# Kernel optimization log

Measured on AMD Instinct MI355X. Metric: run time of the kernel, lower is better.

Reference implementation:

```python
import jax, jax.numpy as jnp
import numpy as np

B, N, C, H = 8, 4096, 768, 8
EPS = 1e-12  # F.normalize eps


def setup_inputs() -> dict:
    key = jax.random.key(0)
    k1, k2, k3, k4 = jax.random.split(key, 4)
    x = jax.random.normal(k1, (B, N, C), dtype=jnp.float32)
    Wqkv = jax.random.normal(k2, (C, 3 * C), dtype=jnp.float32) * (1.0 / np.sqrt(C))
    temperature = jnp.ones((H, 1, 1), dtype=jnp.float32)
    Wproj = jax.random.normal(k3, (C, C), dtype=jnp.float32) * (1.0 / np.sqrt(C))
    bproj = jax.random.normal(k4, (C,), dtype=jnp.float32) * 0.01
    return {"x": x, "Wqkv": Wqkv, "temperature": temperature, "Wproj": Wproj, "bproj": bproj}


def _l2norm(t):
    # F.normalize(dim=-1): t / max(||t||_2, eps)
    n = jnp.sqrt(jnp.sum(t * t, axis=-1, keepdims=True))
    return t / jnp.maximum(n, EPS)


def reference(x, Wqkv, temperature, Wproj, bproj):
    b, n, c = x.shape
    h = temperature.shape[0]
    hd = c // h
    qkv = x @ Wqkv  # [B, N, 3C]
    qkv = qkv.reshape(b, n, 3, h, hd).transpose(2, 0, 3, 4, 1)  # [3, B, H, hd, N]
    q, k, v = qkv[0], qkv[1], qkv[2]
    q = _l2norm(q)  # normalize over token dim N
    k = _l2norm(k)
    # channel-channel attention: [B, H, hd, hd]
    attn = jnp.einsum('bhdn,bhen->bhde', q, k) * temperature  # temperature [H,1,1] broadcasts
    attn = jax.nn.softmax(attn, axis=-1)
    out = jnp.einsum('bhde,bhen->bhdn', attn, v)  # [B, H, hd, N]
    out = out.transpose(0, 3, 1, 2).reshape(b, n, c)  # [B, N, C]
    return out @ Wproj + bproj
```

## Files before the change

kernel.cpp:

```cpp
#include <hip/hip_runtime.h>
#include <stdint.h>


typedef __attribute__((ext_vector_type(8))) __bf16 bf16x8;
typedef __attribute__((ext_vector_type(4))) float f32x4;

__device__ __forceinline__ unsigned short f2b(float f) {
  uint32_t u = __float_as_uint(f);
  u += 0x7FFF + ((u >> 16) & 1);
  return (unsigned short)(u >> 16);
}

__device__ __forceinline__ void gload16(const void* g, void* l) {
  __builtin_amdgcn_global_load_lds(
      (__attribute__((address_space(1))) void*)(uintptr_t)g,
      (__attribute__((address_space(3))) void*)(uintptr_t)l, 16, 0, 0);
}

__global__ void cvt_bf16(const float* __restrict__ in, unsigned short* __restrict__ out, int n4,
                         float* __restrict__ Z, int nz4) {
  int gid = blockIdx.x * blockDim.x + threadIdx.x;
  if (gid < nz4) reinterpret_cast<float4*>(Z)[gid] = make_float4(0.f, 0.f, 0.f, 0.f);
  int stride = gridDim.x * blockDim.x;
  for (int i = gid; i < n4; i += stride) {
    float4 v = reinterpret_cast<const float4*>(in)[i];
    ushort4 o;
    o.x = f2b(v.x); o.y = f2b(v.y); o.z = f2b(v.z); o.w = f2b(v.w);
    reinterpret_cast<ushort4*>(out)[i] = o;
  }
}

__global__ void cvt_transpose(const float* __restrict__ in, unsigned short* __restrict__ out,
                              int K, int NC) {
  __shared__ float tile[32][33];
  int bx = blockIdx.x, by = blockIdx.y;
  int tx = threadIdx.x & 31, ty = threadIdx.x >> 5;
  for (int r = ty; r < 32; r += 8)
    tile[r][tx] = in[(size_t)(by * 32 + r) * NC + bx * 32 + tx];
  __syncthreads();
  for (int r = ty; r < 32; r += 8)
    out[(size_t)(bx * 32 + r) * K + by * 32 + tx] = f2b(tile[tx][r]);
}


#define BARX() asm volatile("s_barrier" ::: "memory")
#define WAITV(N) asm volatile("s_waitcnt vmcnt(" #N ")" ::: "memory")
#define SCHED() __builtin_amdgcn_sched_barrier(0)

#define STAGE(gbase, p, isB, h, t) do {                                             \
  unsigned short* _lb = &lds[(p)*32768 + (isB)*16384 + (h)*8192 + wid*1024];        \
  const unsigned short* _gb = (gbase) + (size_t)((h)*128 + wid*16)*768 + (t)*64 + lanegoff; \
  gload16(_gb, _lb);                                                                \
  gload16(_gb + 8*768, _lb + 512);                                                  \
} while (0)

#define LOAD_A(p, mh) do {                                                          \
  const unsigned short* _ab = &lds[(p)*32768 + (mh)*8192];                          \
  _Pragma("unroll") for (int _mi = 0; _mi < 4; _mi++)                               \
    _Pragma("unroll") for (int _kk = 0; _kk < 2; _kk++)                             \
      af[_mi][_kk] = *(const bf16x8*)&_ab[(wm*64 + _mi*16 + l16)*64 + ((_kk*4+quad)^(l16&7))*8]; \
} while (0)

#define LOAD_B(dst, p, nh) do {                                                     \
  const unsigned short* _bb = &lds[(p)*32768 + 16384 + (nh)*8192];                  \
  _Pragma("unroll") for (int _ni = 0; _ni < 2; _ni++)                               \
    _Pragma("unroll") for (int _kk = 0; _kk < 2; _kk++)                             \
      dst[_ni][_kk] = *(const bf16x8*)&_bb[(wn*32 + _ni*16 + l16)*64 + ((_kk*4+quad)^(l16&7))*8]; \
} while (0)

#define MFMA_PH(mh, nh, bfx) do {                                                   \
  __builtin_amdgcn_s_setprio(1);                                                    \
  _Pragma("unroll") for (int _m = 0; _m < 4; _m++)                                  \
    _Pragma("unroll") for (int _n = 0; _n < 2; _n++)                                \
      _Pragma("unroll") for (int _k = 0; _k < 2; _k++)                              \
        acc[(mh)*4+_m][(nh)*2+_n] = __builtin_amdgcn_mfma_f32_16x16x32_bf16(        \
            af[_m][_k], bfx[_n][_k], acc[(mh)*4+_m][(nh)*2+_n], 0, 0, 0);           \
  __builtin_amdgcn_s_setprio(0);                                                    \
} while (0)

__global__ __launch_bounds__(512, 2) void gemm_qkv(
    const unsigned short* __restrict__ A, const unsigned short* __restrict__ Bt,
    unsigned short* __restrict__ qkT, unsigned short* __restrict__ vT,
    float* __restrict__ normsq) {
  __shared__ __align__(16) unsigned short lds[65536];
  int lin = blockIdx.y * 9 + blockIdx.x;
  int swz = (lin & 7) * 144 + (lin >> 3);
  int bm = swz / 9;
  int bj = swz - bm * 9;
  int m0 = bm * 256, j0 = bj * 256;
  int tid = threadIdx.x;
  int wid = tid >> 6, lane = tid & 63;
  int wm = wid >> 2, wn = wid & 3;
  int quad = lane >> 4, l16 = lane & 15;
  int srow = lane >> 3, sch = lane & 7;
  int cmem = sch ^ srow;
  int lanegoff = srow * 768 + cmem * 8;

  f32x4 acc[8][4];
  f32x4 z = {0.f, 0.f, 0.f, 0.f};
#pragma unroll
  for (int i = 0; i < 8; i++)
#pragma unroll
    for (int j = 0; j < 4; j++) acc[i][j] = z;

  bf16x8 af[4][2], bf0[2][2], bf1[2][2];

  const unsigned short* Ab2 = A + (size_t)m0 * 768;
  const unsigned short* Bb2 = Bt + (size_t)j0 * 768;

  STAGE(Ab2, 0, 0, 0, 0); STAGE(Bb2, 0, 1, 0, 0); STAGE(Bb2, 0, 1, 1, 0); STAGE(Ab2, 0, 0, 1, 0);
  STAGE(Ab2, 1, 0, 0, 1); STAGE(Bb2, 1, 1, 0, 1); STAGE(Bb2, 1, 1, 1, 1);
  WAITV(10);
  BARX();
  LOAD_A(0, 0);
  LOAD_B(bf0, 0, 0);
  WAITV(8);
  BARX();

  for (int t = 0; t < 10; t++) {
    int p = t & 1;
    LOAD_B(bf1, p, 1);
    STAGE(Ab2, p ^ 1, 0, 1, t + 1);
    BARX(); SCHED();
    MFMA_PH(0, 0, bf0);
    SCHED(); WAITV(8); BARX();
    STAGE(Ab2, p, 0, 0, t + 2);
    BARX(); SCHED();
    MFMA_PH(0, 1, bf1);
    SCHED();
    LOAD_A(p, 1);
    BARX();
    STAGE(Bb2, p, 1, 0, t + 2);
    BARX(); SCHED();
    MFMA_PH(1, 1, bf1);
    SCHED(); WAITV(8); BARX();
    STAGE(Bb2, p, 1, 1, t + 2);
    BARX(); SCHED();
    MFMA_PH(1, 0, bf0);
    SCHED();
    LOAD_A(p ^ 1, 0);
    LOAD_B(bf0, p ^ 1, 0);
    WAITV(8); BARX();
  }
  LOAD_B(bf1, 0, 1);
  STAGE(Ab2, 1, 0, 1, 11);
  BARX(); SCHED(); MFMA_PH(0, 0, bf0); SCHED(); WAITV(8); BARX();
  BARX(); SCHED(); MFMA_PH(0, 1, bf1); SCHED(); LOAD_A(0, 1); BARX();
  BARX(); SCHED(); MFMA_PH(1, 1, bf1); SCHED(); WAITV(4); BARX();
  BARX(); SCHED(); MFMA_PH(1, 0, bf0); SCHED(); LOAD_A(1, 0); LOAD_B(bf0, 1, 0); WAITV(2); BARX();
  LOAD_B(bf1, 1, 1);
  BARX(); SCHED(); MFMA_PH(0, 0, bf0); SCHED(); WAITV(0); BARX();
  BARX(); SCHED(); MFMA_PH(0, 1, bf1); SCHED(); LOAD_A(1, 1); BARX();
  BARX(); SCHED(); MFMA_PH(1, 1, bf1); SCHED(); BARX();
  BARX(); SCHED(); MFMA_PH(1, 0, bf0); SCHED(); BARX();

  int s = bj / 3;
  int b = m0 >> 12;
  int n0 = m0 & 4095;

  if (s < 2) {
#pragma unroll
    for (int ni = 0; ni < 4; ni++) {
      float ss = 0.f;
#pragma unroll
      for (int mi = 0; mi < 8; mi++)
#pragma unroll
        for (int r = 0; r < 4; r++) ss += acc[mi][ni][r] * acc[mi][ni][r];
      ss += __shfl_down(ss, 32, 64);
      ss += __shfl_down(ss, 16, 64);
      if (lane < 16) {
        int cc = (ni >> 1) * 128 + wn * 32 + (ni & 1) * 16 + l16;
        int local = j0 + cc - s * 768;
        int hh = local / 96, d = local - hh * 96;
        atomicAdd(&normsq[s * 6144 + (b * 8 + hh) * 96 + d], ss);
      }
    }
#pragma unroll
    for (int jh = 0; jh < 2; jh++) {
      __syncthreads();
#pragma unroll
      for (int nl = 0; nl < 2; nl++) {
        int ni = jh * 2 + nl;
        int jc = wn * 32 + nl * 16 + l16;
#pragma unroll
        for (int mi = 0; mi < 8; mi++) {
          int mrow = (mi >> 2) * 128 + wm * 64 + (mi & 3) * 16 + quad * 4;
#pragma unroll
          for (int r = 0; r < 4; r++) lds[jc * 264 + mrow + r] = f2b(acc[mi][ni][r]);
        }
      }
      __syncthreads();
#pragma unroll
      for (int it = 0; it < 8; it++) {
        int id = it * 512 + tid;
        int jr = id >> 5, mc = id & 31;
        int j = j0 + jh * 128 + jr;
        int local = j - s * 768;
        int hh = local / 96, d = local - hh * 96;
        size_t off = ((size_t)(s * 64 + b * 8 + hh) * 96 + d) * 4096 + n0 + mc * 8;
        *(uint4*)&qkT[off] = *(const uint4*)&lds[jr * 264 + mc * 8];
      }
    }
  } else {
    int j0v = j0 - 1536;
#pragma unroll
    for (int mh = 0; mh < 2; mh++) {
      __syncthreads();
#pragma unroll
      for (int ml = 0; ml < 4; ml++) {
        int mi = mh * 4 + ml;
        int mloc = wm * 64 + ml * 16 + quad * 4;
#pragma unroll
        for (int ni = 0; ni < 4; ni++) {
          int jc = (ni >> 1) * 128 + wn * 32 + (ni & 1) * 16 + l16;
#pragma unroll
          for (int r = 0; r < 4; r++) lds[(mloc + r) * 264 + jc] = f2b(acc[mi][ni][r]);
        }
      }
      __syncthreads();
#pragma unroll
      for (int it = 0; it < 8; it++) {
        int id = it * 512 + tid;
        int mr = id >> 5, ch = id & 31;
        int cp = j0v + ch * 8;
        int hh = cp / 96, e = cp - hh * 96;
        size_t off = ((size_t)(b * 8 + hh) * 4096 + (n0 + mh * 128 + mr)) * 96 + e;
        *(uint4*)&vT[off] = *(const uint4*)&lds[mr * 264 + ch * 8];
      }
    }
  }
}

__global__ __launch_bounds__(256, 2) void attn_s(const unsigned short* __restrict__ qkT,
                                                 float* __restrict__ S) {
  __shared__ __align__(16) unsigned short lds[12288];
  int blk = blockIdx.x;
  int bh = blk >> 3, ks = blk & 7;
  const unsigned short* qb = qkT + (size_t)bh * 96 * 4096;
  const unsigned short* kb = qkT + (size_t)(64 + bh) * 96 * 4096;
  int tid = threadIdx.x, wid = tid >> 6, lane = tid & 63;
  int wm = wid >> 1, wn = wid & 1, quad = lane >> 4, l16 = lane & 15;
  int srow = lane >> 3, sch = lane & 7;
  int cmem = sch ^ srow;
  f32x4 acc[3][3];
  f32x4 z = {0.f, 0.f, 0.f, 0.f};
#pragma unroll
  for (int i = 0; i < 3; i++)
#pragma unroll
    for (int j = 0; j < 3; j++) acc[i][j] = z;

  for (int k0 = ks * 512; k0 < ks * 512 + 512; k0 += 64) {
#pragma unroll
    for (int i = 0; i < 3; i++) {
      int ig = wid * 3 + i;
      int row = ig * 8 + srow;
      gload16(qb + (size_t)row * 4096 + k0 + cmem * 8, &lds[ig * 512]);
      gload16(kb + (size_t)row * 4096 + k0 + cmem * 8, &lds[6144 + ig * 512]);
    }
    __syncthreads();
#pragma unroll
    for (int kk = 0; kk < 2; kk++) {
      int cs = ((kk * 4 + quad) ^ (l16 & 7)) * 8;
      bf16x8 af[3], bfr[3];
#pragma unroll
      for (int mi = 0; mi < 3; mi++)
        af[mi] = *(const bf16x8*)&lds[(wm * 48 + mi * 16 + l16) * 64 + cs];
#pragma unroll
      for (int ni = 0; ni < 3; ni++)
        bfr[ni] = *(const bf16x8*)&lds[6144 + (wn * 48 + ni * 16 + l16) * 64 + cs];
#pragma unroll
      for (int mi = 0; mi < 3; mi++)
#pragma unroll
        for (int ni = 0; ni < 3; ni++)
          acc[mi][ni] = __builtin_amdgcn_mfma_f32_16x16x32_bf16(af[mi], bfr[ni], acc[mi][ni], 0, 0, 0);
    }
    __syncthreads();
  }
  float* Sb = S + (size_t)bh * 9216;
#pragma unroll
  for (int mi = 0; mi < 3; mi++)
#pragma unroll
    for (int ni = 0; ni < 3; ni++)
#pragma unroll
      for (int r = 0; r < 4; r++)
        atomicAdd(&Sb[(wm * 48 + mi * 16 + quad * 4 + r) * 96 + wn * 48 + ni * 16 + l16],
                  acc[mi][ni][r]);
}

__global__ __launch_bounds__(128) void softmax96(
    const float* __restrict__ S, const float* __restrict__ normsq,
    const float* __restrict__ temp, unsigned short* __restrict__ attnB) {
  __shared__ float ik[96];
  int bh = blockIdx.x;
  int h = bh & 7;
  int tid = threadIdx.x;
  if (tid < 96) ik[tid] = 1.0f / fmaxf(sqrtf(normsq[6144 + bh * 96 + tid]), 1e-12f);
  __syncthreads();
  if (tid < 96) {
    int d = tid;
    const float* Srow = S + (size_t)bh * 9216 + d * 96;
    float iq = (1.0f / fmaxf(sqrtf(normsq[bh * 96 + d]), 1e-12f)) * temp[h];
    float mx = -1e30f;
    for (int e = 0; e < 96; e++) mx = fmaxf(mx, Srow[e] * iq * ik[e]);
    float sum = 0.f;
    for (int e = 0; e < 96; e++) sum += __expf(Srow[e] * iq * ik[e] - mx);
    float inv = 1.0f / sum;
    unsigned short* row = attnB + (size_t)bh * 9984 + d * 104;
    for (int e = 0; e < 96; e++) row[e] = f2b(__expf(Srow[e] * iq * ik[e] - mx) * inv);
    for (int e = 96; e < 104; e++) row[e] = 0;
  }
}

__global__ __launch_bounds__(256, 4) void attn_v(
    const unsigned short* __restrict__ attnB, const unsigned short* __restrict__ vT,
    unsigned short* __restrict__ U) {
  __shared__ __align__(16) unsigned short lds[23552];
  int blk = blockIdx.x;
  int bh = blk >> 5, nc = blk & 31;
  int b = bh >> 3, h = bh & 7;
  int n0 = nc * 128;
  int tid = threadIdx.x, wid = tid >> 6, lane = tid & 63;
  int wm = wid >> 1, wn = wid & 1, quad = lane >> 4, l16 = lane & 15;

  const unsigned short* ab = attnB + (size_t)bh * 9984;
#pragma unroll
  for (int i = 0; i < 5; i++) {
    int id = i * 256 + tid;
    int ids = id < 1248 ? id : 1247;
    gload16(ab + (size_t)ids * 8, &lds[(i * 4 + wid) * 512]);
  }

  const unsigned short* vb = vT + (size_t)bh * 4096 * 96 + (size_t)n0 * 96;
#pragma unroll
  for (int i = 0; i < 7; i++) {
    int ig = wid + i * 4;
    if (ig < 26) {
      int id = ig * 64 + lane;
      int row = id / 13;
      int ch = id - row * 13;
      if (ch > 11) ch = 11;
      gload16(vb + (size_t)row * 96 + ch * 8, &lds[10240 + ig * 512]);
    }
  }
  __syncthreads();

  f32x4 acc[3][4];
  f32x4 z = {0.f, 0.f, 0.f, 0.f};
#pragma unroll
  for (int i = 0; i < 3; i++)
#pragma unroll
    for (int j = 0; j < 4; j++) acc[i][j] = z;
#pragma unroll
  for (int et = 0; et < 3; et++) {
    bf16x8 af[3], bfr[4];
#pragma unroll
    for (int mi = 0; mi < 3; mi++)
      af[mi] = *(const bf16x8*)&lds[(wm * 48 + mi * 16 + l16) * 104 + (et * 4 + quad) * 8];
#pragma unroll
    for (int ni = 0; ni < 4; ni++)
      bfr[ni] = *(const bf16x8*)&lds[10240 + (wn * 64 + ni * 16 + l16) * 104 + (et * 4 + quad) * 8];
#pragma unroll
    for (int mi = 0; mi < 3; mi++)
#pragma unroll
      for (int ni = 0; ni < 4; ni++)
        acc[mi][ni] = __builtin_amdgcn_mfma_f32_16x16x32_bf16(af[mi], bfr[ni], acc[mi][ni], 0, 0, 0);
  }
  __syncthreads();

#pragma unroll
  for (int mi = 0; mi < 3; mi++)
#pragma unroll
    for (int ni = 0; ni < 4; ni++)
#pragma unroll
      for (int r = 0; r < 4; r++) {
        int d = wm * 48 + mi * 16 + quad * 4 + r;
        int n = wn * 64 + ni * 16 + l16;
        lds[n * 104 + d] = f2b(acc[mi][ni][r]);
      }
  __syncthreads();
#pragma unroll
  for (int it = 0; it < 6; it++) {
    int id = tid + it * 256;
    int nr = id / 12, ch = id - nr * 12;
    *(uint4*)&U[((size_t)(b * 4096 + n0 + nr)) * 768 + h * 96 + ch * 8] =
        *(const uint4*)&lds[nr * 104 + ch * 8];
  }
}

__global__ __launch_bounds__(256, 2) void gemm_out(
    const unsigned short* __restrict__ A, const unsigned short* __restrict__ Bt,
    const float* __restrict__ bias, float* __restrict__ out) {
  __shared__ __align__(16) unsigned short lds[16384];
  int bj = blockIdx.x;
  int bm = blockIdx.y;
  int m0 = bm * 128, j0 = bj * 128;
  int tid = threadIdx.x;
  int wid = tid >> 6, lane = tid & 63;
  int wm = wid >> 1, wn = wid & 1;
  int quad = lane >> 4, l16 = lane & 15;
  int srow = lane >> 3, sch = lane & 7;
  int cmem = sch ^ srow;

  f32x4 acc[4][4];
  f32x4 z = {0.f, 0.f, 0.f, 0.f};
#pragma unroll
  for (int i = 0; i < 4; i++)
#pragma unroll
    for (int j = 0; j < 4; j++) acc[i][j] = z;

  const unsigned short* Ab = A + (size_t)m0 * 768;
  const unsigned short* Bb = Bt + (size_t)j0 * 768;

  for (int k0 = 0; k0 < 768; k0 += 64) {
#pragma unroll
    for (int i = 0; i < 4; i++) {
      int ig = wid * 4 + i;
      int row = ig * 8 + srow;
      gload16(Ab + (size_t)row * 768 + k0 + cmem * 8, &lds[ig * 512]);
      gload16(Bb + (size_t)row * 768 + k0 + cmem * 8, &lds[8192 + ig * 512]);
    }
    __syncthreads();
#pragma unroll
    for (int kk = 0; kk < 2; kk++) {
      int cs = ((kk * 4 + quad) ^ (l16 & 7)) * 8;
      bf16x8 af[4], bfr[4];
#pragma unroll
      for (int mi = 0; mi < 4; mi++)
        af[mi] = *(const bf16x8*)&lds[(wm * 64 + mi * 16 + l16) * 64 + cs];
#pragma unroll
      for (int ni = 0; ni < 4; ni++)
        bfr[ni] = *(const bf16x8*)&lds[8192 + (wn * 64 + ni * 16 + l16) * 64 + cs];
#pragma unroll
      for (int mi = 0; mi < 4; mi++)
#pragma unroll
        for (int ni = 0; ni < 4; ni++)
          acc[mi][ni] = __builtin_amdgcn_mfma_f32_16x16x32_bf16(af[mi], bfr[ni], acc[mi][ni], 0, 0, 0);
    }
    __syncthreads();
  }
#pragma unroll
  for (int ni = 0; ni < 4; ni++) {
    int ccol = j0 + wn * 64 + ni * 16 + l16;
    float bv = bias[ccol];
#pragma unroll
    for (int mi = 0; mi < 4; mi++)
#pragma unroll
      for (int r = 0; r < 4; r++)
        out[(size_t)(m0 + wm * 64 + mi * 16 + quad * 4 + r) * 768 + ccol] = acc[mi][ni][r] + bv;
  }
}

extern "C" void kernel_launch(void* const* d_in, const int* in_sizes, int n_in,
                              void* d_out, int out_size, void* d_ws, size_t ws_size,
                              hipStream_t stream) {
  const float* x = (const float*)d_in[0];
  const float* Wqkv = (const float*)d_in[1];
  const float* temp = (const float*)d_in[2];
  const float* Wproj = (const float*)d_in[3];
  const float* bproj = (const float*)d_in[4];
  float* out = (float*)d_out;
  char* ws = (char*)d_ws;

  unsigned short* xb     = (unsigned short*)(ws);
  unsigned short* WqkvT  = (unsigned short*)(ws + 50331648);
  unsigned short* WprojT = (unsigned short*)(ws + 53870592);
  unsigned short* qkT    = (unsigned short*)(ws + 55050240);
  unsigned short* vT     = (unsigned short*)(ws + 155713536);
  unsigned short* U      = (unsigned short*)(ws + 206045184);
  float* S               = (float*)(ws + 256376832);
  float* normsq          = (float*)(ws + 258736128);
  unsigned short* attnB  = qkT;

  cvt_bf16<<<dim3(4096), dim3(256), 0, stream>>>(x, xb, 25165824 / 4, S, 150528);
  cvt_transpose<<<dim3(72, 24), dim3(256), 0, stream>>>(Wqkv, WqkvT, 768, 2304);
  cvt_transpose<<<dim3(24, 24), dim3(256), 0, stream>>>(Wproj, WprojT, 768, 768);
  gemm_qkv<<<dim3(9, 128), dim3(512), 0, stream>>>(xb, WqkvT, qkT, vT, normsq);
  attn_s<<<dim3(512), dim3(256), 0, stream>>>(qkT, S);
  softmax96<<<dim3(64), dim3(128), 0, stream>>>(S, normsq, temp, attnB);
  attn_v<<<dim3(2048), dim3(256), 0, stream>>>(attnB, vT, U);
  gemm_out<<<dim3(6, 256), dim3(256), 0, stream>>>(U, WprojT, bproj, out);
}
```

Before: 434.4 us.

## Replace atomic split-K reduction with partial buffers and parallelize softmax

attn_s now writes each K-split's partial 96x96 score tile to its own slice of a workspace buffer, which reuses the xb region since xb is no longer needed at that point, instead of accumulating into S with atomicAdd. The softmax kernel sums the 8 partials itself and runs on a 4x64 grid of 256-thread blocks, one wave per row with shuffle reductions, replacing the old 64 blocks with one thread per row. This drops the atomic traffic and the S zeroing, and raises softmax parallelism. The cost is extra partial-buffer writes and reads.

```diff
diff --git a/kernel.cpp b/kernel.cpp
--- a/kernel.cpp
+++ b/kernel.cpp
@@ -232,7 +232,7 @@
 }
 
 __global__ __launch_bounds__(256, 2) void attn_s(const unsigned short* __restrict__ qkT,
-                                                 float* __restrict__ S) {
+                                                 float* __restrict__ S8) {
   __shared__ __align__(16) unsigned short lds[12288];
   int blk = blockIdx.x;
   int bh = blk >> 3, ks = blk & 7;
@@ -276,38 +276,61 @@
     }
     __syncthreads();
   }
-  float* Sb = S + (size_t)bh * 9216;
+  float* Sb = S8 + ((size_t)ks * 64 + bh) * 9216;
 #pragma unroll
   for (int mi = 0; mi < 3; mi++)
 #pragma unroll
     for (int ni = 0; ni < 3; ni++)
 #pragma unroll
       for (int r = 0; r < 4; r++)
-        atomicAdd(&Sb[(wm * 48 + mi * 16 + quad * 4 + r) * 96 + wn * 48 + ni * 16 + l16],
-                  acc[mi][ni][r]);
-}
-
-__global__ __launch_bounds__(128) void softmax96(
-    const float* __restrict__ S, const float* __restrict__ normsq,
+        Sb[(wm * 48 + mi * 16 + quad * 4 + r) * 96 + wn * 48 + ni * 16 + l16] = acc[mi][ni][r];
+}
+
+__global__ __launch_bounds__(256) void softmax96(
+    const float* __restrict__ S8, const float* __restrict__ normsq,
     const float* __restrict__ temp, unsigned short* __restrict__ attnB) {
-  __shared__ float ik[96];
-  int bh = blockIdx.x;
+  __shared__ float Sl[24][97];
+  __shared__ float ik[96], iqv[24];
+  int part = blockIdx.x;
+  int bh = blockIdx.y;
   int h = bh & 7;
+  int base = part * 24;
   int tid = threadIdx.x;
-  if (tid < 96) ik[tid] = 1.0f / fmaxf(sqrtf(normsq[6144 + bh * 96 + tid]), 1e-12f);
+  if (tid < 96) {
+    ik[tid] = 1.0f / fmaxf(sqrtf(normsq[6144 + bh * 96 + tid]), 1e-12f);
+  } else if (tid >= 128 && tid < 152) {
+    int d = base + tid - 128;
+    iqv[tid - 128] = (1.0f / fmaxf(sqrtf(normsq[bh * 96 + d]), 1e-12f)) * temp[h];
+  }
+  const float* Sbase = S8 + (size_t)bh * 9216 + base * 96;
+#pragma unroll
+  for (int i = 0; i < 9; i++) {
+    int idx = i * 256 + tid;
+    int r = idx / 96, e = idx - r * 96;
+    float s = 0.f;
+#pragma unroll
+    for (int ksb = 0; ksb < 8; ksb++) s += Sbase[(size_t)ksb * 589824 + r * 96 + e];
+    Sl[r][e] = s;
+  }
   __syncthreads();
-  if (tid < 96) {
-    int d = tid;
-    const float* Srow = S + (size_t)bh * 9216 + d * 96;
-    float iq = (1.0f / fmaxf(sqrtf(normsq[bh * 96 + d]), 1e-12f)) * temp[h];
-    float mx = -1e30f;
-    for (int e = 0; e < 96; e++) mx = fmaxf(mx, Srow[e] * iq * ik[e]);
-    float sum = 0.f;
-    for (int e = 0; e < 96; e++) sum += __expf(Srow[e] * iq * ik[e] - mx);
-    float inv = 1.0f / sum;
-    unsigned short* row = attnB + (size_t)bh * 9984 + d * 104;
-    for (int e = 0; e < 96; e++) row[e] = f2b(__expf(Srow[e] * iq * ik[e] - mx) * inv);
-    for (int e = 96; e < 104; e++) row[e] = 0;
+  int wv = tid >> 6, lane = tid & 63;
+  for (int r = wv; r < 24; r += 4) {
+    float iq = iqv[r];
+    float v0 = Sl[r][lane] * iq * ik[lane];
+    float v1 = (lane < 32) ? Sl[r][64 + lane] * iq * ik[64 + lane] : -1e30f;
+    float mx = fmaxf(v0, v1);
+#pragma unroll
+    for (int off = 32; off; off >>= 1) mx = fmaxf(mx, __shfl_xor(mx, off, 64));
+    float e0 = __expf(v0 - mx);
+    float e1 = (lane < 32) ? __expf(v1 - mx) : 0.f;
+    float sm = e0 + e1;
+#pragma unroll
+    for (int off = 32; off; off >>= 1) sm += __shfl_xor(sm, off, 64);
+    float inv = 1.0f / sm;
+    unsigned short* row = attnB + (size_t)bh * 9984 + (base + r) * 104;
+    row[lane] = f2b(e0 * inv);
+    if (lane < 32) row[64 + lane] = f2b(e1 * inv);
+    else if (64 + lane < 104) row[64 + lane] = 0;
   }
 }
 
@@ -467,16 +490,16 @@
   unsigned short* qkT    = (unsigned short*)(ws + 55050240);
   unsigned short* vT     = (unsigned short*)(ws + 155713536);
   unsigned short* U      = (unsigned short*)(ws + 206045184);
-  float* S               = (float*)(ws + 256376832);
   float* normsq          = (float*)(ws + 258736128);
+  float* S8              = (float*)(ws);
   unsigned short* attnB  = qkT;
 
-  cvt_bf16<<<dim3(4096), dim3(256), 0, stream>>>(x, xb, 25165824 / 4, S, 150528);
+  cvt_bf16<<<dim3(4096), dim3(256), 0, stream>>>(x, xb, 25165824 / 4, normsq, 3072);
   cvt_transpose<<<dim3(72, 24), dim3(256), 0, stream>>>(Wqkv, WqkvT, 768, 2304);
   cvt_transpose<<<dim3(24, 24), dim3(256), 0, stream>>>(Wproj, WprojT, 768, 768);
   gemm_qkv<<<dim3(9, 128), dim3(512), 0, stream>>>(xb, WqkvT, qkT, vT, normsq);
-  attn_s<<<dim3(512), dim3(256), 0, stream>>>(qkT, S);
-  softmax96<<<dim3(64), dim3(128), 0, stream>>>(S, normsq, temp, attnB);
+  attn_s<<<dim3(512), dim3(256), 0, stream>>>(qkT, S8);
+  softmax96<<<dim3(4, 64), dim3(256), 0, stream>>>(S8, normsq, temp, attnB);
   attn_v<<<dim3(2048), dim3(256), 0, stream>>>(attnB, vT, U);
   gemm_out<<<dim3(6, 256), dim3(256), 0, stream>>>(U, WprojT, bproj, out);
 }
```

Measured after the change: 426.4 us. No clear change (-1.9%).
